# Kernel optimization log

Measured on AMD Instinct MI355X. Metric: run time of the kernel, lower is better.

The kernel has to match this reference:

```python
import jax, jax.numpy as jnp
import numpy as np

D = 512
B, S = 4, 4096


def setup_inputs() -> dict:
    key = jax.random.key(0)
    ks = jax.random.split(key, 8)
    scale = 1.0 / np.sqrt(D)
    return {
        "x": jax.random.normal(ks[0], (B, S, D), dtype=jnp.float32),
        "bias": jax.random.normal(ks[1], (1, S, S), dtype=jnp.float32),
        "Wq_w": jax.random.normal(ks[2], (D, D), dtype=jnp.float32) * scale,
        "Wq_b": jax.random.normal(ks[3], (D,), dtype=jnp.float32) * 0.02,
        "Wk_w": jax.random.normal(ks[4], (D, D), dtype=jnp.float32) * scale,
        "Wk_b": jax.random.normal(ks[5], (D,), dtype=jnp.float32) * 0.02,
        "Wv_w": jax.random.normal(ks[6], (D, D), dtype=jnp.float32) * scale,
        "Wv_b": jax.random.normal(ks[7], (D,), dtype=jnp.float32) * 0.02,
    }


def reference(x, bias, Wq_w, Wq_b, Wk_w, Wk_b, Wv_w, Wv_b):
    # torch nn.Linear: y = x @ W.T + b
    q = jnp.einsum("bsd,ed->bse", x, Wq_w) + Wq_b
    k = jnp.einsum("bsd,ed->bse", x, Wk_w) + Wk_b
    v = jnp.einsum("bsd,ed->bse", x, Wv_w) + Wv_b
    inv_sqrt_d = jnp.asarray(1.0 / np.sqrt(D), dtype=x.dtype)
    # scores: [B, S, S] -- scale by sqrt(feature_dim) as in the original
    scores = jnp.einsum("bqd,bkd->bqk", q * inv_sqrt_d, k) + bias
    weights = jax.nn.sigmoid(scores)
    out = jnp.einsum("bqk,bkd->bqd", weights, v)
    return out
```

## Files before the change

### kernel.cpp

```cpp
#include <hip/hip_runtime.h>
#include <hip/hip_bf16.h>
#include <stdint.h>

typedef unsigned short bf16_t;
typedef __attribute__((ext_vector_type(4))) short s4v;
typedef __attribute__((ext_vector_type(8))) short short8;
typedef __attribute__((ext_vector_type(4))) float f32x4;

__device__ __forceinline__ bf16_t f2b(float f) {
    union { float f; uint32_t u; } v; v.f = f;
    uint32_t u = v.u;
    return (bf16_t)((u + 0x7FFFu + ((u >> 16) & 1u)) >> 16);
}

__global__ __launch_bounds__(256) void cvt_f32_bf16(const float* __restrict__ in,
                                                    bf16_t* __restrict__ out, int n4) {
    int i = blockIdx.x * blockDim.x + threadIdx.x;
    if (i >= n4) return;
    float4 f = ((const float4*)in)[i];
    ushort4 o;
    o.x = f2b(f.x); o.y = f2b(f.y); o.z = f2b(f.z); o.w = f2b(f.w);
    ((ushort4*)out)[i] = o;
}

__global__ __launch_bounds__(256) void cvt_w3(const float* __restrict__ a,
                                              const float* __restrict__ b,
                                              const float* __restrict__ c,
                                              bf16_t* __restrict__ out) {
    int i = blockIdx.x * blockDim.x + threadIdx.x;
    const int which = i >> 16;
    const int idx   = i & 65535;
    const float* src = (which == 0) ? a : (which == 1) ? b : c;
    float4 f = ((const float4*)src)[idx];
    ushort4 o;
    o.x = f2b(f.x); o.y = f2b(f.y); o.z = f2b(f.z); o.w = f2b(f.w);
    ((ushort4*)out)[i] = o;
}

__device__ __forceinline__ void lds_dma16(const void* g, void* l) {
    __builtin_amdgcn_global_load_lds(
        (const __attribute__((address_space(1))) void*)g,
        (__attribute__((address_space(3))) void*)l, 16, 0, 0);
}


__global__ __launch_bounds__(256)
void proj_all(const bf16_t* __restrict__ Xb, const bf16_t* __restrict__ Wb,
              const float* __restrict__ qb, const float* __restrict__ kb,
              const float* __restrict__ vb,
              bf16_t* __restrict__ Qb, bf16_t* __restrict__ Kb,
              bf16_t* __restrict__ Vt)
{
    __shared__ __align__(16) bf16_t lds[2][16384];

    const int tid  = threadIdx.x;
    const int lane = tid & 63;
    const int w    = tid >> 6;
    const int wm   = w & 1, wn = w >> 1;
    const int ll   = lane & 15;
    const int quad = lane >> 4;

    const int bid   = blockIdx.x;
    const int x     = bid & 7;
    const int g     = bid >> 3;
    const int mi    = x * 16 + g / 12;
    const int inner = g % 12;
    const int m0 = mi * 128;
    const int n0 = (inner & 3) * 128;
    const int z  = inner >> 2;

    const bf16_t* A = Xb;
    const bf16_t* B = Wb + z * 262144;

    auto stage = [&](int kt, int b) {
#pragma unroll
        for (int c = 0; c < 4; ++c) {
            const int base = (c * 4 + w) * 64;
            const int slot = base + lane;
            const int row  = slot >> 3;
            const int kc   = ((slot & 7) ^ (row & 7)) << 3;
            lds_dma16(A + (size_t)(m0 + row) * 512 + kt * 64 + kc, (char*)&lds[b][0]    + base * 16);
            lds_dma16(B + (size_t)(n0 + row) * 512 + kt * 64 + kc, (char*)&lds[b][8192] + base * 16);
        }
    };

    f32x4 acc[4][4];
#pragma unroll
    for (int i = 0; i < 4; i++)
#pragma unroll
        for (int j = 0; j < 4; j++) acc[i][j] = (f32x4){0.f, 0.f, 0.f, 0.f};

    stage(0, 0);
    __syncthreads();
    int cur = 0;
    for (int kt = 0; kt < 8; ++kt) {
        if (kt < 7) stage(kt + 1, cur ^ 1);
        const bf16_t* lsA = &lds[cur][0];
        const bf16_t* lsB = &lds[cur][8192];
#pragma unroll
        for (int t = 0; t < 2; t++) {
            short8 af[4], bf[4];
#pragma unroll
            for (int i = 0; i < 4; i++) {
                const int ri = wm * 64 + i * 16 + ll;
                const int rj = wn * 64 + i * 16 + ll;
                af[i] = *(const short8*)(lsA + ri * 64 + (((t * 4 + quad) ^ (ll & 7)) << 3));
                bf[i] = *(const short8*)(lsB + rj * 64 + (((t * 4 + quad) ^ (ll & 7)) << 3));
            }
#pragma unroll
            for (int i = 0; i < 4; i++)
#pragma unroll
                for (int j = 0; j < 4; j++)
                    acc[i][j] = __builtin_amdgcn_mfma_f32_16x16x32_bf16(af[i], bf[j], acc[i][j], 0, 0, 0);
        }
        __syncthreads();
        cur ^= 1;
    }

    bf16_t* wbuf = &lds[0][0] + w * 4096;
    const float inv = 0.044194173824159216f;

    if (z != 2) {
        const float* bptr = (z == 0) ? qb : kb;
        const float scl   = (z == 0) ? inv : 1.0f;
#pragma unroll
        for (int j = 0; j < 4; j++) {
            const int colL = j * 16 + ll;
            const float bv = bptr[n0 + wn * 64 + colL];
#pragma unroll
            for (int i = 0; i < 4; i++) {
                f32x4 a = acc[i][j];
#pragma unroll
                for (int r = 0; r < 4; r++) {
                    const int rowL = i * 16 + quad * 4 + r;
                    wbuf[rowL * 64 + (colL ^ ((rowL & 7) << 3))] = f2b((a[r] + bv) * scl);
                }
            }
        }
        __syncthreads();
        bf16_t* dst = (z == 0) ? Qb : Kb;
        const int rowg0 = m0 + wm * 64;
        const int colg0 = n0 + wn * 64;
#pragma unroll
        for (int k = 0; k < 8; k++) {
            const int rowL = (lane >> 3) + k * 8;
            const int c0   = (lane & 7) * 8;
            short8 vv = *(const short8*)(wbuf + rowL * 64 + (c0 ^ ((rowL & 7) << 3)));
            *(short8*)(dst + (size_t)(rowg0 + rowL) * 512 + colg0 + c0) = vv;
        }
    } else {
#pragma unroll
        for (int j = 0; j < 4; j++) {
            const int d = j * 16 + ll;
            const float bv = vb[n0 + wn * 64 + d];
#pragma unroll
            for (int i = 0; i < 4; i++) {
                f32x4 a = acc[i][j];
                s4v pk;
                pk[0] = (short)f2b(a[0] + bv);
                pk[1] = (short)f2b(a[1] + bv);
                pk[2] = (short)f2b(a[2] + bv);
                pk[3] = (short)f2b(a[3] + bv);
                const int sB = i * 16 + quad * 4;
                *(s4v*)(wbuf + d * 64 + (sB ^ ((d & 7) << 3))) = pk;
            }
        }
        __syncthreads();
        const int rowg0 = m0 + wm * 64;
        const int b  = rowg0 >> 12;
        const int s0 = rowg0 & 4095;
        const int d0 = n0 + wn * 64;
#pragma unroll
        for (int k = 0; k < 8; k++) {
            const int dL = (lane >> 3) + k * 8;
            const int c0 = (lane & 7) * 8;
            short8 vv = *(const short8*)(wbuf + dL * 64 + (c0 ^ ((dL & 7) << 3)));
            *(short8*)(Vt + ((size_t)b * 512 + d0 + dL) * 4096 + s0 + c0) = vv;
        }
    }
}

__global__ __launch_bounds__(256)
void scores_sig(const bf16_t* __restrict__ Qb, const bf16_t* __restrict__ Kb,
                const float* __restrict__ bias, bf16_t* __restrict__ P)
{
    __shared__ __align__(16) bf16_t lds[2][16384];

    const int tid  = threadIdx.x;
    const int lane = tid & 63;
    const int w    = tid >> 6;
    const int wm   = w & 1, wn = w >> 1;
    const int ll   = lane & 15;
    const int quad = lane >> 4;

    const int bx  = blockIdx.x;
    const int z   = bx & 3;
    const int t_  = bx >> 2;
    const int sup = t_ >> 5;
    const int win = t_ & 31;
    const int m0  = ((sup >> 2) * 4 + (win & 3)) * 128;
    const int n0  = ((sup & 3) * 8 + (win >> 2)) * 128;

    const bf16_t* A = Qb + (size_t)z * 2097152;
    const bf16_t* B = Kb + (size_t)z * 2097152;
    bf16_t* out = P + (size_t)z * 16777216;

    auto stage = [&](int kt, int b) {
#pragma unroll
        for (int c = 0; c < 4; ++c) {
            const int base = (c * 4 + w) * 64;
            const int slot = base + lane;
            const int row  = slot >> 3;
            const int kc   = ((slot & 7) ^ (row & 7)) << 3;
            lds_dma16(A + (size_t)(m0 + row) * 512 + kt * 64 + kc, (char*)&lds[b][0]    + base * 16);
            lds_dma16(B + (size_t)(n0 + row) * 512 + kt * 64 + kc, (char*)&lds[b][8192] + base * 16);
        }
    };

    f32x4 acc[4][4];
#pragma unroll
    for (int i = 0; i < 4; i++)
#pragma unroll
        for (int j = 0; j < 4; j++) acc[i][j] = (f32x4){0.f, 0.f, 0.f, 0.f};

    stage(0, 0);
    __syncthreads();
    int cur = 0;
    for (int kt = 0; kt < 8; ++kt) {
        if (kt < 7) stage(kt + 1, cur ^ 1);
        const bf16_t* lsA = &lds[cur][0];
        const bf16_t* lsB = &lds[cur][8192];
#pragma unroll
        for (int t = 0; t < 2; t++) {
            short8 af[4], bf[4];
#pragma unroll
            for (int i = 0; i < 4; i++) {
                const int ri = wm * 64 + i * 16 + ll;
                const int rj = wn * 64 + i * 16 + ll;
                af[i] = *(const short8*)(lsA + ri * 64 + (((t * 4 + quad) ^ (ll & 7)) << 3));
                bf[i] = *(const short8*)(lsB + rj * 64 + (((t * 4 + quad) ^ (ll & 7)) << 3));
            }
#pragma unroll
            for (int i = 0; i < 4; i++)
#pragma unroll
                for (int j = 0; j < 4; j++)
                    acc[i][j] = __builtin_amdgcn_mfma_f32_16x16x32_bf16(af[i], bf[j], acc[i][j], 0, 0, 0);
        }
        __syncthreads();
        cur ^= 1;
    }

#pragma unroll
    for (int i = 0; i < 4; i++) {
#pragma unroll
        for (int j = 0; j < 4; j++) {
            const int col  = n0 + wn * 64 + j * 16 + ll;
            const int rowb = m0 + wm * 64 + i * 16 + quad * 4;
            f32x4 a = acc[i][j];
#pragma unroll
            for (int r = 0; r < 4; r++) {
                const int row = rowb + r;
                const float v = a[r] + bias[(size_t)row * 4096 + col];
                const float p = __builtin_amdgcn_rcpf(1.f + __expf(-v));
                out[(size_t)row * 4096 + col] = (bf16_t)(__float_as_uint(p) >> 16);
            }
        }
    }
}

__global__ __launch_bounds__(256)
void pv_gemm(const bf16_t* __restrict__ P, const bf16_t* __restrict__ Vt,
             float* __restrict__ outg)
{
    __shared__ __align__(16) bf16_t lds[2][16384];

    const int tid  = threadIdx.x;
    const int lane = tid & 63;
    const int w    = tid >> 6;
    const int wm   = w & 1, wn = w >> 1;
    const int ll   = lane & 15;
    const int quad = lane >> 4;

    const int n0 = blockIdx.x * 128;
    const int m0 = blockIdx.y * 128;
    const int z  = blockIdx.z;

    const bf16_t* A = P + (size_t)z * 16777216;
    const bf16_t* B = Vt + (size_t)z * 2097152;
    float* out = outg + (size_t)z * 2097152;

    auto stage = [&](int kt, int b) {
#pragma unroll
        for (int c = 0; c < 4; ++c) {
            const int base = (c * 4 + w) * 64;
            const int slot = base + lane;
            const int row  = slot >> 3;
            const int kc   = ((slot & 7) ^ (row & 7)) << 3;
            lds_dma16(A + (size_t)(m0 + row) * 4096 + kt * 64 + kc, (char*)&lds[b][0]    + base * 16);
            lds_dma16(B + (size_t)(n0 + row) * 4096 + kt * 64 + kc, (char*)&lds[b][8192] + base * 16);
        }
    };

    f32x4 acc[4][4];
#pragma unroll
    for (int i = 0; i < 4; i++)
#pragma unroll
        for (int j = 0; j < 4; j++) acc[i][j] = (f32x4){0.f, 0.f, 0.f, 0.f};

    stage(0, 0);
    __syncthreads();
    int cur = 0;
    for (int kt = 0; kt < 64; ++kt) {
        if (kt < 63) stage(kt + 1, cur ^ 1);
        const bf16_t* lsA = &lds[cur][0];
        const bf16_t* lsB = &lds[cur][8192];
#pragma unroll
        for (int t = 0; t < 2; t++) {
            short8 af[4], bf[4];
#pragma unroll
            for (int i = 0; i < 4; i++) {
                const int ri = wm * 64 + i * 16 + ll;
                const int rj = wn * 64 + i * 16 + ll;
                af[i] = *(const short8*)(lsA + ri * 64 + (((t * 4 + quad) ^ (ll & 7)) << 3));
                bf[i] = *(const short8*)(lsB + rj * 64 + (((t * 4 + quad) ^ (ll & 7)) << 3));
            }
#pragma unroll
            for (int i = 0; i < 4; i++)
#pragma unroll
                for (int j = 0; j < 4; j++)
                    acc[i][j] = __builtin_amdgcn_mfma_f32_16x16x32_bf16(af[i], bf[j], acc[i][j], 0, 0, 0);
        }
        __syncthreads();
        cur ^= 1;
    }

#pragma unroll
    for (int i = 0; i < 4; i++) {
#pragma unroll
        for (int j = 0; j < 4; j++) {
            const int col  = n0 + wn * 64 + j * 16 + ll;
            const int rowb = m0 + wm * 64 + i * 16 + quad * 4;
            f32x4 a = acc[i][j];
#pragma unroll
            for (int r = 0; r < 4; r++)
                out[(size_t)(rowb + r) * 512 + col] = a[r];
        }
    }
}

extern "C" void kernel_launch(void* const* d_in, const int* in_sizes, int n_in,
                              void* d_out, int out_size, void* d_ws, size_t ws_size,
                              hipStream_t stream) {
    (void)in_sizes; (void)n_in; (void)out_size; (void)ws_size;
    const float* x    = (const float*)d_in[0];
    const float* bias = (const float*)d_in[1];
    const float* Wq_w = (const float*)d_in[2];
    const float* Wq_b = (const float*)d_in[3];
    const float* Wk_w = (const float*)d_in[4];
    const float* Wk_b = (const float*)d_in[5];
    const float* Wv_w = (const float*)d_in[6];
    const float* Wv_b = (const float*)d_in[7];
    float* out = (float*)d_out;

    bf16_t* Xb = (bf16_t*)d_ws;
    bf16_t* Wb = Xb + (size_t)16384 * 512;
    bf16_t* Qb = Wb + (size_t)3 * 512 * 512;
    bf16_t* Kb = Qb + (size_t)16384 * 512;
    bf16_t* Vt = Kb + (size_t)16384 * 512;
    bf16_t* P  = Vt + (size_t)16384 * 512;

    cvt_f32_bf16<<<8192, 256, 0, stream>>>(x, Xb, 2097152);
    cvt_w3<<<768, 256, 0, stream>>>(Wq_w, Wk_w, Wv_w, Wb);

    proj_all<<<1536, 256, 0, stream>>>(Xb, Wb, Wq_b, Wk_b, Wv_b, Qb, Kb, Vt);
    scores_sig<<<4096, 256, 0, stream>>>(Qb, Kb, bias, P);
    pv_gemm<<<dim3(4, 32, 4), 256, 0, stream>>>(P, Vt, out);
}
```

Measured before the change: 386.5 us.

## Convert bias to bf16 and retile PV GEMM to full-width 32-row blocks

Adds a pass that converts the fp32 bias matrix to bf16 into the output buffer, so the scores kernel reads half the bias bytes on each of its four per-batch passes. The PV GEMM is restructured to 512-thread blocks covering 32 rows by all 512 output columns, staging the whole V tile per k-step. Double buffering is dropped, so loads no longer overlap compute, and V traffic per block increases. Bias precision is reduced to bf16.

```diff
diff --git a/kernel.cpp b/kernel.cpp
--- a/kernel.cpp
+++ b/kernel.cpp
@@ -11,6 +11,12 @@
     union { float f; uint32_t u; } v; v.f = f;
     uint32_t u = v.u;
     return (bf16_t)((u + 0x7FFFu + ((u >> 16) & 1u)) >> 16);
+}
+
+__device__ __forceinline__ float b2f(bf16_t b) {
+    union { uint32_t u; float f; } v;
+    v.u = ((uint32_t)b) << 16;
+    return v.f;
 }
 
 __global__ __launch_bounds__(256) void cvt_f32_bf16(const float* __restrict__ in,
@@ -182,8 +188,9 @@
 
 __global__ __launch_bounds__(256)
 void scores_sig(const bf16_t* __restrict__ Qb, const bf16_t* __restrict__ Kb,
-                const float* __restrict__ bias, bf16_t* __restrict__ P)
+                const bf16_t* __restrict__ biasб, bf16_t* __restrict__ P)
 {
+    const bf16_t* __restrict__ biasb = biasб;
     __shared__ __align__(16) bf16_t lds[2][16384];
 
     const int tid  = threadIdx.x;
@@ -260,7 +267,7 @@
 #pragma unroll
             for (int r = 0; r < 4; r++) {
                 const int row = rowb + r;
-                const float v = a[r] + bias[(size_t)row * 4096 + col];
+                const float v = a[r] + b2f(biasb[(size_t)row * 4096 + col]);
                 const float p = __builtin_amdgcn_rcpf(1.f + __expf(-v));
                 out[(size_t)row * 4096 + col] = (bf16_t)(__float_as_uint(p) >> 16);
             }
@@ -268,78 +275,76 @@
     }
 }
 
-__global__ __launch_bounds__(256)
+__global__ __launch_bounds__(512)
 void pv_gemm(const bf16_t* __restrict__ P, const bf16_t* __restrict__ Vt,
              float* __restrict__ outg)
 {
-    __shared__ __align__(16) bf16_t lds[2][16384];
+    __shared__ __align__(16) bf16_t lsA[32 * 64];
+    __shared__ __align__(16) bf16_t lsB[512 * 64];
 
     const int tid  = threadIdx.x;
     const int lane = tid & 63;
     const int w    = tid >> 6;
-    const int wm   = w & 1, wn = w >> 1;
     const int ll   = lane & 15;
     const int quad = lane >> 4;
 
-    const int n0 = blockIdx.x * 128;
-    const int m0 = blockIdx.y * 128;
-    const int z  = blockIdx.z;
+    const int m0 = blockIdx.x * 32;
+    const int z  = blockIdx.y;
 
     const bf16_t* A = P + (size_t)z * 16777216;
     const bf16_t* B = Vt + (size_t)z * 2097152;
     float* out = outg + (size_t)z * 2097152;
 
-    auto stage = [&](int kt, int b) {
-#pragma unroll
-        for (int c = 0; c < 4; ++c) {
-            const int base = (c * 4 + w) * 64;
-            const int slot = base + lane;
+    f32x4 acc[2][4];
+#pragma unroll
+    for (int i = 0; i < 2; i++)
+#pragma unroll
+        for (int j = 0; j < 4; j++) acc[i][j] = (f32x4){0.f, 0.f, 0.f, 0.f};
+
+    for (int k0 = 0; k0 < 4096; k0 += 64) {
+        if (tid < 256) {
+            const int slot = tid;
             const int row  = slot >> 3;
             const int kc   = ((slot & 7) ^ (row & 7)) << 3;
-            lds_dma16(A + (size_t)(m0 + row) * 4096 + kt * 64 + kc, (char*)&lds[b][0]    + base * 16);
-            lds_dma16(B + (size_t)(n0 + row) * 4096 + kt * 64 + kc, (char*)&lds[b][8192] + base * 16);
-        }
-    };
-
-    f32x4 acc[4][4];
-#pragma unroll
-    for (int i = 0; i < 4; i++)
-#pragma unroll
-        for (int j = 0; j < 4; j++) acc[i][j] = (f32x4){0.f, 0.f, 0.f, 0.f};
-
-    stage(0, 0);
-    __syncthreads();
-    int cur = 0;
-    for (int kt = 0; kt < 64; ++kt) {
-        if (kt < 63) stage(kt + 1, cur ^ 1);
-        const bf16_t* lsA = &lds[cur][0];
-        const bf16_t* lsB = &lds[cur][8192];
+            lds_dma16(A + (size_t)(m0 + row) * 4096 + k0 + kc, (char*)lsA + slot * 16);
+        }
+#pragma unroll
+        for (int c = 0; c < 8; ++c) {
+            const int slot = c * 512 + tid;
+            const int row  = slot >> 3;
+            const int kc   = ((slot & 7) ^ (row & 7)) << 3;
+            lds_dma16(B + (size_t)row * 4096 + k0 + kc, (char*)lsB + slot * 16);
+        }
+        __syncthreads();
+
 #pragma unroll
         for (int t = 0; t < 2; t++) {
-            short8 af[4], bf[4];
-#pragma unroll
-            for (int i = 0; i < 4; i++) {
-                const int ri = wm * 64 + i * 16 + ll;
-                const int rj = wn * 64 + i * 16 + ll;
+            short8 af[2], bf[4];
+#pragma unroll
+            for (int i = 0; i < 2; i++) {
+                const int ri = i * 16 + ll;
                 af[i] = *(const short8*)(lsA + ri * 64 + (((t * 4 + quad) ^ (ll & 7)) << 3));
-                bf[i] = *(const short8*)(lsB + rj * 64 + (((t * 4 + quad) ^ (ll & 7)) << 3));
-            }
-#pragma unroll
-            for (int i = 0; i < 4; i++)
+            }
+#pragma unroll
+            for (int j = 0; j < 4; j++) {
+                const int rj = w * 64 + j * 16 + ll;
+                bf[j] = *(const short8*)(lsB + rj * 64 + (((t * 4 + quad) ^ (ll & 7)) << 3));
+            }
+#pragma unroll
+            for (int i = 0; i < 2; i++)
 #pragma unroll
                 for (int j = 0; j < 4; j++)
                     acc[i][j] = __builtin_amdgcn_mfma_f32_16x16x32_bf16(af[i], bf[j], acc[i][j], 0, 0, 0);
         }
         __syncthreads();
-        cur ^= 1;
-    }
-
-#pragma unroll
-    for (int i = 0; i < 4; i++) {
+    }
+
+#pragma unroll
+    for (int i = 0; i < 2; i++) {
 #pragma unroll
         for (int j = 0; j < 4; j++) {
-            const int col  = n0 + wn * 64 + j * 16 + ll;
-            const int rowb = m0 + wm * 64 + i * 16 + quad * 4;
+            const int col  = w * 64 + j * 16 + ll;
+            const int rowb = m0 + i * 16 + quad * 4;
             f32x4 a = acc[i][j];
 #pragma unroll
             for (int r = 0; r < 4; r++)
@@ -368,11 +373,13 @@
     bf16_t* Kb = Qb + (size_t)16384 * 512;
     bf16_t* Vt = Kb + (size_t)16384 * 512;
     bf16_t* P  = Vt + (size_t)16384 * 512;
+    bf16_t* Bb = (bf16_t*)d_out;
 
     cvt_f32_bf16<<<8192, 256, 0, stream>>>(x, Xb, 2097152);
     cvt_w3<<<768, 256, 0, stream>>>(Wq_w, Wk_w, Wv_w, Wb);
+    cvt_f32_bf16<<<16384, 256, 0, stream>>>(bias, Bb, 4194304);
 
     proj_all<<<1536, 256, 0, stream>>>(Xb, Wb, Wq_b, Wk_b, Wv_b, Qb, Kb, Vt);
-    scores_sig<<<4096, 256, 0, stream>>>(Qb, Kb, bias, P);
-    pv_gemm<<<dim3(4, 32, 4), 256, 0, stream>>>(P, Vt, out);
-}
+    scores_sig<<<4096, 256, 0, stream>>>(Qb, Kb, Bb, P);
+    pv_gemm<<<dim3(128, 4), 512, 0, stream>>>(P, Vt, out);
+}
```

Result: slower. 400.8 us (+3.7%).

## Pre-convert bias to bf16 inside projection launch and read it in scores

Applied to the files above, without the earlier changes.

Adds 2048 extra blocks to the projection kernel that convert the 4096x4096 fp32 bias to bf16, staging it in the output buffer. The scores kernel then reads the bf16 bias instead of fp32. Each of the 4 batch slices of scores reads the bias again, so this is meant to halve that repeated traffic. In exchange it adds one full fp32 read plus a bf16 write of the bias, and rounds the bias to bf16 before it enters the sigmoid.

```diff
diff --git a/kernel.cpp b/kernel.cpp
--- a/kernel.cpp
+++ b/kernel.cpp
@@ -11,6 +11,12 @@
     union { float f; uint32_t u; } v; v.f = f;
     uint32_t u = v.u;
     return (bf16_t)((u + 0x7FFFu + ((u >> 16) & 1u)) >> 16);
+}
+
+__device__ __forceinline__ float b2f(bf16_t b) {
+    union { uint32_t u; float f; } v;
+    v.u = ((uint32_t)b) << 16;
+    return v.f;
 }
 
 __global__ __launch_bounds__(256) void cvt_f32_bf16(const float* __restrict__ in,
@@ -49,18 +55,33 @@
               const float* __restrict__ qb, const float* __restrict__ kb,
               const float* __restrict__ vb,
               bf16_t* __restrict__ Qb, bf16_t* __restrict__ Kb,
-              bf16_t* __restrict__ Vt)
+              bf16_t* __restrict__ Vt,
+              const float* __restrict__ biasf, bf16_t* __restrict__ biasb)
 {
     __shared__ __align__(16) bf16_t lds[2][16384];
 
     const int tid  = threadIdx.x;
+    const int bid  = blockIdx.x;
+
+    if (bid >= 1536) {
+        const int base = (bid - 1536) * 256 + tid;
+#pragma unroll
+        for (int k = 0; k < 8; ++k) {
+            const int i = base + k * 524288;
+            float4 f = ((const float4*)biasf)[i];
+            ushort4 o;
+            o.x = f2b(f.x); o.y = f2b(f.y); o.z = f2b(f.z); o.w = f2b(f.w);
+            ((ushort4*)biasb)[i] = o;
+        }
+        return;
+    }
+
     const int lane = tid & 63;
     const int w    = tid >> 6;
     const int wm   = w & 1, wn = w >> 1;
     const int ll   = lane & 15;
     const int quad = lane >> 4;
 
-    const int bid   = blockIdx.x;
     const int x     = bid & 7;
     const int g     = bid >> 3;
     const int mi    = x * 16 + g / 12;
@@ -182,7 +203,7 @@
 
 __global__ __launch_bounds__(256)
 void scores_sig(const bf16_t* __restrict__ Qb, const bf16_t* __restrict__ Kb,
-                const float* __restrict__ bias, bf16_t* __restrict__ P)
+                const bf16_t* __restrict__ biasb, bf16_t* __restrict__ P)
 {
     __shared__ __align__(16) bf16_t lds[2][16384];
 
@@ -260,7 +281,7 @@
 #pragma unroll
             for (int r = 0; r < 4; r++) {
                 const int row = rowb + r;
-                const float v = a[r] + bias[(size_t)row * 4096 + col];
+                const float v = a[r] + b2f(biasb[(size_t)row * 4096 + col]);
                 const float p = __builtin_amdgcn_rcpf(1.f + __expf(-v));
                 out[(size_t)row * 4096 + col] = (bf16_t)(__float_as_uint(p) >> 16);
             }
@@ -368,11 +389,13 @@
     bf16_t* Kb = Qb + (size_t)16384 * 512;
     bf16_t* Vt = Kb + (size_t)16384 * 512;
     bf16_t* P  = Vt + (size_t)16384 * 512;
+    bf16_t* Bb = (bf16_t*)d_out;
 
     cvt_f32_bf16<<<8192, 256, 0, stream>>>(x, Xb, 2097152);
     cvt_w3<<<768, 256, 0, stream>>>(Wq_w, Wk_w, Wv_w, Wb);
 
-    proj_all<<<1536, 256, 0, stream>>>(Xb, Wb, Wq_b, Wk_b, Wv_b, Qb, Kb, Vt);
-    scores_sig<<<4096, 256, 0, stream>>>(Qb, Kb, bias, P);
+    proj_all<<<3584, 256, 0, stream>>>(Xb, Wb, Wq_b, Wk_b, Wv_b, Qb, Kb, Vt,
+                                       bias, Bb);
+    scores_sig<<<4096, 256, 0, stream>>>(Qb, Kb, Bb, P);
     pv_gemm<<<dim3(4, 32, 4), 256, 0, stream>>>(P, Vt, out);
 }
```

After: 391.5 us. About the same (+1.3%).
